# Optimization experiments

Hardware: AMD Instinct MI355X
Metric: run time of the kernel (lower is better)

The kernel has to match this reference:

```python
import jax, jax.numpy as jnp
import numpy as np

VNUM = 50000
OUT = 128
E = 1600000
EPS = 1e-7


def setup_inputs() -> dict:
    key = jax.random.key(0)
    k = jax.random.split(key, 8)
    sidx = jax.random.randint(k[0], (E,), 0, VNUM, dtype=jnp.int64 if jax.config.jax_enable_x64 else jnp.int32)
    tidx = jax.random.randint(k[1], (E,), 0, VNUM, dtype=sidx.dtype)
    enorm = jax.random.uniform(k[2], (E,), dtype=jnp.float32)
    # edge signs +-1 as in signed graph conv
    esgn = jnp.where(jax.random.uniform(k[3], (E,)) < 0.5, -1.0, 1.0).astype(jnp.float32)
    # vrepr initialized trunc_normal(std=0.1) (zero_init=False)
    vrepr = 0.1 * jax.random.truncated_normal(k[4], -2.0, 2.0, (VNUM, OUT), dtype=jnp.float32)
    lim = 1.0 / np.sqrt(OUT)
    loc_w = jax.random.uniform(k[5], (OUT, OUT), jnp.float32, -lim, lim)
    loc_b = jnp.zeros((OUT,), jnp.float32)
    std_w = jax.random.uniform(k[6], (OUT, OUT), jnp.float32, -lim, lim)
    std_b = jnp.zeros((OUT,), jnp.float32)
    return {"sidx": sidx, "tidx": tidx, "enorm": enorm, "esgn": esgn,
            "vrepr": vrepr, "loc_w": loc_w, "loc_b": loc_b,
            "std_w": std_w, "std_b": std_b}


def reference(sidx, tidx, enorm, esgn, vrepr, loc_w, loc_b, std_w, std_b):
    # GraphConv: edge-weighted gather + scatter-add aggregation
    msg = vrepr[sidx] * (esgn * enorm)[:, None]          # [E, OUT]
    ptr = jax.ops.segment_sum(msg, tidx, num_segments=VNUM)  # [VNUM, OUT]
    loc = ptr @ loc_w.T + loc_b                          # Normal loc
    std = jax.nn.softplus(ptr @ std_w.T + std_b) + EPS   # Normal scale
    return loc, std
```

## Files before the change

### kernel.cpp

```cpp
#include <hip/hip_runtime.h>
#include <math.h>

#define VNUM 50000
#define OUTF 128
#define NEDGE 1600000
#define EPSF 1e-7f

#define CONV_BLOCKS 6250
#define BFRAG_BLOCKS 64

#define CHUNK 2048
#define NCB 49
#define COARSE_BLOCKS 782
#define NSUB 4
#define FINE_BLOCKS (NCB * NSUB)

typedef __attribute__((ext_vector_type(8))) short short8;
typedef __attribute__((ext_vector_type(4))) float v4f;

__device__ __forceinline__ unsigned short f2bf(float f) {
    union { float f; unsigned int u; } c; c.f = f;
    unsigned int u = c.u;
    return (unsigned short)((u + 0x7FFFu + ((u >> 16) & 1u)) >> 16);
}
__device__ __forceinline__ float bf16_lo(unsigned int p) {
    union { unsigned int u; float f; } c; c.u = p << 16; return c.f;
}
__device__ __forceinline__ float bf16_hi(unsigned int p) {
    union { unsigned int u; float f; } c; c.u = p & 0xFFFF0000u; return c.f;
}

__device__ __forceinline__ int wave_incl_scan(int v, int lane) {
#pragma unroll
    for (int off = 1; off < 64; off <<= 1) {
        const int o = __shfl_up(v, off, 64);
        if (lane >= off) v += o;
    }
    return v;
}

__global__ __launch_bounds__(256) void prep_kernel(
    const float* __restrict__ vrepr, unsigned int* __restrict__ vrepr16,
    const int* __restrict__ tidx, int* __restrict__ chist,
    const float* __restrict__ loc_w, const float* __restrict__ std_w,
    unsigned int* bfrag)
{
    __shared__ int lc[4][NCB];
    const int b = blockIdx.x, tid = threadIdx.x;
    if (b < CONV_BLOCKS) {
        const size_t base = (size_t)b * 1024 + tid * 4;
        const float4 v = *reinterpret_cast<const float4*>(vrepr + base);
        uint2 o;
        o.x = (unsigned)f2bf(v.x) | ((unsigned)f2bf(v.y) << 16);
        o.y = (unsigned)f2bf(v.z) | ((unsigned)f2bf(v.w) << 16);
        *reinterpret_cast<uint2*>(vrepr16 + base / 2) = o;
    } else if (b < CONV_BLOCKS + COARSE_BLOCKS) {
        const int hb = b - CONV_BLOCKS;
        for (int i = tid; i < 4 * NCB; i += 256) (&lc[0][0])[i] = 0;
        __syncthreads();
        const int base = hb * CHUNK;
#pragma unroll
        for (int j = 0; j < 8; ++j) {
            const int e = base + j * 256 + tid;
            if (e < NEDGE) atomicAdd(&lc[tid >> 6][tidx[e] >> 10], 1);
        }
        __syncthreads();
        if (tid < NCB) {
            const int s = lc[0][tid] + lc[1][tid] + lc[2][tid] + lc[3][tid];
            if (s) atomicAdd(&chist[tid], s);
        }
    } else {
        const int p = (b - (CONV_BLOCKS + COARSE_BLOCKS)) * 256 + tid;
        const int j2 = p & 3, lq = (p >> 2) & 63, ks = (p >> 8) & 3, ct = p >> 10;
        const int k = ks * 32 + (lq >> 4) * 8 + j2 * 2;
        const int n = ct * 16 + (lq & 15);
        const float* wsrc = (n >> 7) ? std_w : loc_w;
        const int c = n & 127;
        bfrag[p] = (unsigned)f2bf(wsrc[c * 128 + k]) |
                   ((unsigned)f2bf(wsrc[c * 128 + k + 1]) << 16);
    }
}

__global__ __launch_bounds__(64) void scan_coarse_kernel(
    const int* __restrict__ chist, int* __restrict__ cbase,
    int* __restrict__ ccursor, int* __restrict__ offs)
{
    const int tid = threadIdx.x;
    const int v = (tid < NCB) ? chist[tid] : 0;
    const int inc = wave_incl_scan(v, tid);
    const int ex = inc - v;
    if (tid < NCB) { cbase[tid] = ex; ccursor[tid] = ex; }
    if (tid == NCB - 1) { cbase[NCB] = inc; offs[VNUM] = inc; }
}

__global__ __launch_bounds__(256) void coarse_kernel(
    const int* __restrict__ sidx, const int* __restrict__ tidx,
    const float* __restrict__ enorm, const float* __restrict__ esgn,
    int* __restrict__ ccursor, uint2* __restrict__ coarse8)
{
    __shared__ uint2 lrec[CHUNK];
    __shared__ int lcnt[4][NCB];
    __shared__ int lbase[4][NCB];
    __shared__ int loffs[NCB];
    __shared__ int grun[NCB];

    const int tid = threadIdx.x, lane = tid & 63, wv = tid >> 6;
    const int base = blockIdx.x * CHUNK;
    const int n = min(CHUNK, NEDGE - base);

    for (int i = tid; i < 4 * NCB; i += 256) (&lcnt[0][0])[i] = 0;
    __syncthreads();

    uint2 rec[8];
#pragma unroll
    for (int j = 0; j < 8; ++j) {
        const int e = base + j * 256 + tid;
        if (e < NEDGE) {
            const int t = tidx[e];
            const float w = esgn[e] * enorm[e];
            rec[j].x = ((unsigned)sidx[e] << 16) | (unsigned)f2bf(w);
            rec[j].y = (unsigned)t;
            atomicAdd(&lcnt[wv][t >> 10], 1);
        }
    }
    __syncthreads();

    if (tid < 64) {
        int c0 = 0, c1 = 0, c2 = 0, c3 = 0, tot = 0;
        if (lane < NCB) {
            c0 = lcnt[0][lane]; c1 = lcnt[1][lane];
            c2 = lcnt[2][lane]; c3 = lcnt[3][lane];
            tot = c0 + c1 + c2 + c3;
        }
        const int inc = wave_incl_scan(tot, lane);
        const int ex = inc - tot;
        if (lane < NCB) {
            loffs[lane]    = ex;
            lbase[0][lane] = ex;
            lbase[1][lane] = ex + c0;
            lbase[2][lane] = ex + c0 + c1;
            lbase[3][lane] = ex + c0 + c1 + c2;
            grun[lane] = atomicAdd(&ccursor[lane], tot);
        }
    }
    __syncthreads();

#pragma unroll
    for (int j = 0; j < 8; ++j) {
        const int e = base + j * 256 + tid;
        if (e < NEDGE) {
            const int cb = (int)(rec[j].y >> 10);
            const int pos = atomicAdd(&lbase[wv][cb], 1);
            lrec[pos] = rec[j];
        }
    }
    __syncthreads();

    for (int i = tid; i < n; i += 256) {
        const uint2 r = lrec[i];
        const int cb = (int)(r.y >> 10);
        coarse8[grun[cb] + (i - loffs[cb])] = r;
    }
}

__global__ __launch_bounds__(1024) void hist_kernel(
    const uint2* __restrict__ coarse8, const int* __restrict__ cbase,
    int* __restrict__ hcnt)
{
    __shared__ int cnt[1024];
    const int tid = threadIdx.x;
    const int bin = blockIdx.x >> 2, s = blockIdx.x & 3;
    const int s0 = cbase[bin], len = cbase[bin + 1] - s0;
    const int qs = s0 + ((len * s) >> 2);
    const int qe = s0 + ((len * (s + 1)) >> 2);
    cnt[tid] = 0;
    __syncthreads();
    for (int i = qs + tid; i < qe; i += 1024)
        atomicAdd(&cnt[coarse8[i].y & 1023], 1);
    __syncthreads();
    hcnt[blockIdx.x * 1024 + tid] = cnt[tid];
}

__global__ __launch_bounds__(1024) void scatter_fine_kernel(
    const uint2* __restrict__ coarse8, const int* __restrict__ cbase,
    const int* __restrict__ hcnt, int* __restrict__ offs,
    unsigned int* __restrict__ pairs)
{
    __shared__ int cur[1024];
    __shared__ int wsum[16];
    const int tid = threadIdx.x, lane = tid & 63, wv = tid >> 6;
    const int bin = blockIdx.x >> 2, s = blockIdx.x & 3;
    const int s0 = cbase[bin], len = cbase[bin + 1] - s0;
    const int qs = s0 + ((len * s) >> 2);
    const int qe = s0 + ((len * (s + 1)) >> 2);

    const int c0 = hcnt[(bin * 4 + 0) * 1024 + tid];
    const int c1 = hcnt[(bin * 4 + 1) * 1024 + tid];
    const int c2 = hcnt[(bin * 4 + 2) * 1024 + tid];
    const int c3 = hcnt[(bin * 4 + 3) * 1024 + tid];
    const int tot = c0 + c1 + c2 + c3;
    const int pre = (s > 0 ? c0 : 0) + (s > 1 ? c1 : 0) + (s > 2 ? c2 : 0);

    const int inc = wave_incl_scan(tot, lane);
    if (lane == 63) wsum[wv] = inc;
    __syncthreads();
    if (tid == 0) {
        int run = 0;
        for (int i = 0; i < 16; ++i) { const int t = wsum[i]; wsum[i] = run; run += t; }
    }
    __syncthreads();
    const int ex = s0 + wsum[wv] + inc - tot;
    const int gv = (bin << 10) + tid;
    if (s == 0 && gv < VNUM) offs[gv] = ex;
    cur[tid] = ex + pre;
    __syncthreads();

    for (int i = qs + tid; i < qe; i += 1024) {
        const uint2 r = coarse8[i];
        const int pos = atomicAdd(&cur[r.y & 1023], 1);
        pairs[pos] = r.x;
    }
}

__global__ __launch_bounds__(256) void aggregate_kernel(
    const int* __restrict__ offs, const unsigned int* __restrict__ pairs,
    const unsigned int* __restrict__ vrepr16, float* __restrict__ acc)
{
    const int v = blockIdx.x * 4 + (threadIdx.x >> 6);
    const int l = threadIdx.x & 63;
    int i = offs[v];
    const int end = offs[v + 1];

    float a0 = 0.0f, a1 = 0.0f;
    for (; i + 8 <= end; i += 8) {
        unsigned p[8], r[8];
#pragma unroll
        for (int j = 0; j < 8; ++j) p[j] = pairs[i + j];
#pragma unroll
        for (int j = 0; j < 8; ++j) r[j] = vrepr16[(size_t)(p[j] >> 16) * 64 + l];
#pragma unroll
        for (int j = 0; j < 8; ++j) {
            const float w = bf16_lo(p[j]);
            a0 = fmaf(bf16_lo(r[j]), w, a0);
            a1 = fmaf(bf16_hi(r[j]), w, a1);
        }
    }
    for (; i + 4 <= end; i += 4) {
        const unsigned p0 = pairs[i], p1 = pairs[i + 1];
        const unsigned p2 = pairs[i + 2], p3 = pairs[i + 3];
        const unsigned r0 = vrepr16[(size_t)(p0 >> 16) * 64 + l];
        const unsigned r1 = vrepr16[(size_t)(p1 >> 16) * 64 + l];
        const unsigned r2 = vrepr16[(size_t)(p2 >> 16) * 64 + l];
        const unsigned r3 = vrepr16[(size_t)(p3 >> 16) * 64 + l];
        const float w0 = bf16_lo(p0), w1 = bf16_lo(p1);
        const float w2 = bf16_lo(p2), w3 = bf16_lo(p3);
        a0 = fmaf(bf16_lo(r0), w0, a0); a1 = fmaf(bf16_hi(r0), w0, a1);
        a0 = fmaf(bf16_lo(r1), w1, a0); a1 = fmaf(bf16_hi(r1), w1, a1);
        a0 = fmaf(bf16_lo(r2), w2, a0); a1 = fmaf(bf16_hi(r2), w2, a1);
        a0 = fmaf(bf16_lo(r3), w3, a0); a1 = fmaf(bf16_hi(r3), w3, a1);
    }
    for (; i < end; ++i) {
        const unsigned p = pairs[i];
        const unsigned r = vrepr16[(size_t)(p >> 16) * 64 + l];
        const float w = bf16_lo(p);
        a0 = fmaf(bf16_lo(r), w, a0); a1 = fmaf(bf16_hi(r), w, a1);
    }
    *reinterpret_cast<float2*>(acc + (size_t)v * OUTF + 2 * l) = make_float2(a0, a1);
}

__global__ __launch_bounds__(256) void gemm_mfma_kernel(
    const float* acc, const unsigned int* __restrict__ bfrag,
    const float* __restrict__ loc_b, const float* __restrict__ std_b,
    float* out)
{
    __shared__ unsigned short tile[16][136];
    const int t = threadIdx.x;
    const int row0 = blockIdx.x * 16;
    const int l = t & 63, w = t >> 6;

    short8 bfr[4][4];
#pragma unroll
    for (int ct = 0; ct < 4; ++ct)
#pragma unroll
        for (int ks = 0; ks < 4; ++ks)
            bfr[ct][ks] = *reinterpret_cast<const short8*>(
                bfrag + ((((w * 4 + ct) * 4 + ks) * 64 + l) << 2));

    {
        const float* src = acc + (size_t)row0 * OUTF + t * 8;
        const float4 v0 = *reinterpret_cast<const float4*>(src);
        const float4 v1 = *reinterpret_cast<const float4*>(src + 4);
        uint4 pk;
        pk.x = (unsigned)f2bf(v0.x) | ((unsigned)f2bf(v0.y) << 16);
        pk.y = (unsigned)f2bf(v0.z) | ((unsigned)f2bf(v0.w) << 16);
        pk.z = (unsigned)f2bf(v1.x) | ((unsigned)f2bf(v1.y) << 16);
        pk.w = (unsigned)f2bf(v1.z) | ((unsigned)f2bf(v1.w) << 16);
        *reinterpret_cast<uint4*>(&tile[t >> 4][(t & 15) * 8]) = pk;
    }
    __syncthreads();

    const int m = l & 15, q = l >> 4;
    v4f accv[4];
#pragma unroll
    for (int ct = 0; ct < 4; ++ct) accv[ct] = (v4f){0.0f, 0.0f, 0.0f, 0.0f};

#pragma unroll
    for (int ks = 0; ks < 4; ++ks) {
        const short8 a = *reinterpret_cast<const short8*>(&tile[m][ks * 32 + q * 8]);
#pragma unroll
        for (int ct = 0; ct < 4; ++ct)
            accv[ct] = __builtin_amdgcn_mfma_f32_16x16x32_bf16(
                a, bfr[ct][ks], accv[ct], 0, 0, 0);
    }

#pragma unroll
    for (int ct = 0; ct < 4; ++ct) {
        const int colg = (w * 4 + ct) * 16 + m;
        const int h = colg >> 7, c = colg & 127;
        const float bias = (h ? std_b : loc_b)[c];
        float* dst = out + (h ? (size_t)VNUM * OUTF : (size_t)0);
#pragma unroll
        for (int reg = 0; reg < 4; ++reg) {
            const int row = row0 + q * 4 + reg;
            float x = accv[ct][reg] + bias;
            if (h) x = fmaxf(x, 0.0f) + log1pf(expf(-fabsf(x))) + EPSF;
            dst[(size_t)row * OUTF + c] = x;
        }
    }
}

__global__ __launch_bounds__(256) void gemm_fallback_kernel(
    const float* acc,
    const float* __restrict__ loc_w, const float* __restrict__ loc_b,
    const float* __restrict__ std_w, const float* __restrict__ std_b,
    float* out)
{
    __shared__ float tile[16][OUTF];
    const int t = threadIdx.x;
    const int row0 = blockIdx.x * 16;
    {
        const float4* src = reinterpret_cast<const float4*>(acc + (size_t)row0 * OUTF);
        float4* dst = reinterpret_cast<float4*>(&tile[0][0]);
        dst[t] = src[t]; dst[t + 256] = src[t + 256];
    }
    __syncthreads();
    const int is_std = t >> 7;
    const int c = t & 127;
    const float* w = (is_std ? std_w : loc_w) + (size_t)c * OUTF;
    const float bias = is_std ? std_b[c] : loc_b[c];
    float accv[16];
#pragma unroll
    for (int r = 0; r < 16; ++r) accv[r] = 0.0f;
    for (int k = 0; k < OUTF; k += 4) {
        const float4 wv = *reinterpret_cast<const float4*>(w + k);
#pragma unroll
        for (int r = 0; r < 16; ++r) {
            const float4 pv = *reinterpret_cast<const float4*>(&tile[r][k]);
            float a = accv[r];
            a = fmaf(pv.x, wv.x, a); a = fmaf(pv.y, wv.y, a);
            a = fmaf(pv.z, wv.z, a); a = fmaf(pv.w, wv.w, a);
            accv[r] = a;
        }
    }
    float* dst_base = out + (is_std ? (size_t)VNUM * OUTF : (size_t)0);
#pragma unroll
    for (int r = 0; r < 16; ++r) {
        const float x = accv[r] + bias;
        dst_base[(size_t)(row0 + r) * OUTF + c] =
            is_std ? (fmaxf(x, 0.0f) + log1pf(expf(-fabsf(x))) + EPSF) : x;
    }
}

extern "C" void kernel_launch(void* const* d_in, const int* in_sizes, int n_in,
                              void* d_out, int out_size, void* d_ws, size_t ws_size,
                              hipStream_t stream) {
    const int*   sidx  = (const int*)  d_in[0];
    const int*   tidx  = (const int*)  d_in[1];
    const float* enorm = (const float*)d_in[2];
    const float* esgn  = (const float*)d_in[3];
    const float* vrepr = (const float*)d_in[4];
    const float* loc_w = (const float*)d_in[5];
    const float* loc_b = (const float*)d_in[6];
    const float* std_w = (const float*)d_in[7];
    const float* std_b = (const float*)d_in[8];

    float* out = (float*)d_out;

    uint2* coarse8 = (uint2*)out;

    unsigned int* sbase   = (unsigned int*)(out + (size_t)VNUM * OUTF);
    unsigned int* pairs   = sbase;
    unsigned int* vrepr16 = sbase + NEDGE;
    int* offs    = (int*)(sbase + NEDGE + (size_t)VNUM * 64);
    int* cbase   = offs + VNUM + 1;
    int* ccursor = cbase + NCB + 1;
    int* chist   = ccursor + NCB;
    int* hcnt    = chist + NCB;

    const bool use_ws = ws_size >= 16384 * sizeof(unsigned int);
    unsigned int* bfrag = use_ws ? (unsigned int*)d_ws : nullptr;

    hipMemsetAsync(chist, 0, NCB * sizeof(int), stream);

    const int prep_blocks = CONV_BLOCKS + COARSE_BLOCKS + (use_ws ? BFRAG_BLOCKS : 0);
    prep_kernel       <<<prep_blocks, 256, 0, stream>>>(vrepr, vrepr16, tidx, chist,
                                                        loc_w, std_w, bfrag);
    scan_coarse_kernel<<<1, 64, 0, stream>>>(chist, cbase, ccursor, offs);
    coarse_kernel     <<<COARSE_BLOCKS, 256, 0, stream>>>(sidx, tidx, enorm, esgn,
                                                          ccursor, coarse8);
    hist_kernel       <<<FINE_BLOCKS, 1024, 0, stream>>>(coarse8, cbase, hcnt);
    scatter_fine_kernel<<<FINE_BLOCKS, 1024, 0, stream>>>(coarse8, cbase, hcnt,
                                                          offs, pairs);

    float* acc = out;
    aggregate_kernel<<<VNUM / 4, 256, 0, stream>>>(offs, pairs, vrepr16, acc);

    if (use_ws) {
        gemm_mfma_kernel<<<VNUM / 16, 256, 0, stream>>>(acc, bfrag, loc_b, std_b, out);
    } else {
        gemm_fallback_kernel<<<VNUM / 16, 256, 0, stream>>>(acc, loc_w, loc_b,
                                                            std_w, std_b, out);
    }
}
```

Measured before the change: 253.3 us.

## Replace coarse histogram pre-pass with fixed-stride bin slots and post-scan

Each coarse bin gets a fixed-capacity region (BSTRIDE) in the staging buffer, so the atomic cursors start at fixed offsets. This removes the tidx histogram pass, the memset and the pre-scan. A small scan after coarse binning derives the compacted offsets from the final cursor values. The aggregate loop also gains a 12-way unrolled gather for more memory-level parallelism. The change risks overflow if any bin exceeds the fixed capacity under skewed target distributions.

```diff
diff --git a/kernel.cpp b/kernel.cpp
--- a/kernel.cpp
+++ b/kernel.cpp
@@ -12,6 +12,7 @@
 #define CHUNK 2048
 #define NCB 49
 #define COARSE_BLOCKS 782
+#define BSTRIDE 36864
 #define NSUB 4
 #define FINE_BLOCKS (NCB * NSUB)
 
@@ -41,11 +42,10 @@
 
 __global__ __launch_bounds__(256) void prep_kernel(
     const float* __restrict__ vrepr, unsigned int* __restrict__ vrepr16,
-    const int* __restrict__ tidx, int* __restrict__ chist,
+    int* __restrict__ ccursor,
     const float* __restrict__ loc_w, const float* __restrict__ std_w,
     unsigned int* bfrag)
 {
-    __shared__ int lc[4][NCB];
     const int b = blockIdx.x, tid = threadIdx.x;
     if (b < CONV_BLOCKS) {
         const size_t base = (size_t)b * 1024 + tid * 4;
@@ -54,23 +54,10 @@
         o.x = (unsigned)f2bf(v.x) | ((unsigned)f2bf(v.y) << 16);
         o.y = (unsigned)f2bf(v.z) | ((unsigned)f2bf(v.w) << 16);
         *reinterpret_cast<uint2*>(vrepr16 + base / 2) = o;
-    } else if (b < CONV_BLOCKS + COARSE_BLOCKS) {
-        const int hb = b - CONV_BLOCKS;
-        for (int i = tid; i < 4 * NCB; i += 256) (&lc[0][0])[i] = 0;
-        __syncthreads();
-        const int base = hb * CHUNK;
-#pragma unroll
-        for (int j = 0; j < 8; ++j) {
-            const int e = base + j * 256 + tid;
-            if (e < NEDGE) atomicAdd(&lc[tid >> 6][tidx[e] >> 10], 1);
-        }
-        __syncthreads();
-        if (tid < NCB) {
-            const int s = lc[0][tid] + lc[1][tid] + lc[2][tid] + lc[3][tid];
-            if (s) atomicAdd(&chist[tid], s);
-        }
+    } else if (b == CONV_BLOCKS) {
+        if (tid < NCB) ccursor[tid] = tid * BSTRIDE;
     } else {
-        const int p = (b - (CONV_BLOCKS + COARSE_BLOCKS)) * 256 + tid;
+        const int p = (b - (CONV_BLOCKS + 1)) * 256 + tid;
         const int j2 = p & 3, lq = (p >> 2) & 63, ks = (p >> 8) & 3, ct = p >> 10;
         const int k = ks * 32 + (lq >> 4) * 8 + j2 * 2;
         const int n = ct * 16 + (lq & 15);
@@ -79,18 +66,6 @@
         bfrag[p] = (unsigned)f2bf(wsrc[c * 128 + k]) |
                    ((unsigned)f2bf(wsrc[c * 128 + k + 1]) << 16);
     }
-}
-
-__global__ __launch_bounds__(64) void scan_coarse_kernel(
-    const int* __restrict__ chist, int* __restrict__ cbase,
-    int* __restrict__ ccursor, int* __restrict__ offs)
-{
-    const int tid = threadIdx.x;
-    const int v = (tid < NCB) ? chist[tid] : 0;
-    const int inc = wave_incl_scan(v, tid);
-    const int ex = inc - v;
-    if (tid < NCB) { cbase[tid] = ex; ccursor[tid] = ex; }
-    if (tid == NCB - 1) { cbase[NCB] = inc; offs[VNUM] = inc; }
 }
 
 __global__ __launch_bounds__(256) void coarse_kernel(
@@ -163,6 +138,18 @@
     }
 }
 
+__global__ __launch_bounds__(64) void scan_mid_kernel(
+    const int* __restrict__ ccursor, int* __restrict__ cbase,
+    int* __restrict__ offs)
+{
+    const int tid = threadIdx.x;
+    const int len = (tid < NCB) ? (ccursor[tid] - tid * BSTRIDE) : 0;
+    const int inc = wave_incl_scan(len, tid);
+    const int ex = inc - len;
+    if (tid < NCB) cbase[tid] = ex;
+    if (tid == NCB - 1) { cbase[NCB] = inc; offs[VNUM] = inc; }
+}
+
 __global__ __launch_bounds__(1024) void hist_kernel(
     const uint2* __restrict__ coarse8, const int* __restrict__ cbase,
     int* __restrict__ hcnt)
@@ -170,9 +157,10 @@
     __shared__ int cnt[1024];
     const int tid = threadIdx.x;
     const int bin = blockIdx.x >> 2, s = blockIdx.x & 3;
-    const int s0 = cbase[bin], len = cbase[bin + 1] - s0;
-    const int qs = s0 + ((len * s) >> 2);
-    const int qe = s0 + ((len * (s + 1)) >> 2);
+    const int bs = bin * BSTRIDE;
+    const int len = cbase[bin + 1] - cbase[bin];
+    const int qs = bs + ((len * s) >> 2);
+    const int qe = bs + ((len * (s + 1)) >> 2);
     cnt[tid] = 0;
     __syncthreads();
     for (int i = qs + tid; i < qe; i += 1024)
@@ -190,9 +178,11 @@
     __shared__ int wsum[16];
     const int tid = threadIdx.x, lane = tid & 63, wv = tid >> 6;
     const int bin = blockIdx.x >> 2, s = blockIdx.x & 3;
-    const int s0 = cbase[bin], len = cbase[bin + 1] - s0;
-    const int qs = s0 + ((len * s) >> 2);
-    const int qe = s0 + ((len * (s + 1)) >> 2);
+    const int bs = bin * BSTRIDE;
+    const int s0 = cbase[bin];
+    const int len = cbase[bin + 1] - s0;
+    const int qs = bs + ((len * s) >> 2);
+    const int qe = bs + ((len * (s + 1)) >> 2);
 
     const int c0 = hcnt[(bin * 4 + 0) * 1024 + tid];
     const int c1 = hcnt[(bin * 4 + 1) * 1024 + tid];
@@ -232,6 +222,19 @@
     const int end = offs[v + 1];
 
     float a0 = 0.0f, a1 = 0.0f;
+    for (; i + 12 <= end; i += 12) {
+        unsigned p[12], r[12];
+#pragma unroll
+        for (int j = 0; j < 12; ++j) p[j] = pairs[i + j];
+#pragma unroll
+        for (int j = 0; j < 12; ++j) r[j] = vrepr16[(size_t)(p[j] >> 16) * 64 + l];
+#pragma unroll
+        for (int j = 0; j < 12; ++j) {
+            const float w = bf16_lo(p[j]);
+            a0 = fmaf(bf16_lo(r[j]), w, a0);
+            a1 = fmaf(bf16_hi(r[j]), w, a1);
+        }
+    }
     for (; i + 8 <= end; i += 8) {
         unsigned p[8], r[8];
 #pragma unroll
@@ -394,20 +397,17 @@
     int* offs    = (int*)(sbase + NEDGE + (size_t)VNUM * 64);
     int* cbase   = offs + VNUM + 1;
     int* ccursor = cbase + NCB + 1;
-    int* chist   = ccursor + NCB;
-    int* hcnt    = chist + NCB;
+    int* hcnt    = ccursor + NCB;
 
     const bool use_ws = ws_size >= 16384 * sizeof(unsigned int);
     unsigned int* bfrag = use_ws ? (unsigned int*)d_ws : nullptr;
 
-    hipMemsetAsync(chist, 0, NCB * sizeof(int), stream);
-
-    const int prep_blocks = CONV_BLOCKS + COARSE_BLOCKS + (use_ws ? BFRAG_BLOCKS : 0);
-    prep_kernel       <<<prep_blocks, 256, 0, stream>>>(vrepr, vrepr16, tidx, chist,
+    const int prep_blocks = CONV_BLOCKS + 1 + (use_ws ? BFRAG_BLOCKS : 0);
+    prep_kernel       <<<prep_blocks, 256, 0, stream>>>(vrepr, vrepr16, ccursor,
                                                         loc_w, std_w, bfrag);
-    scan_coarse_kernel<<<1, 64, 0, stream>>>(chist, cbase, ccursor, offs);
     coarse_kernel     <<<COARSE_BLOCKS, 256, 0, stream>>>(sidx, tidx, enorm, esgn,
                                                           ccursor, coarse8);
+    scan_mid_kernel   <<<1, 64, 0, stream>>>(ccursor, cbase, offs);
     hist_kernel       <<<FINE_BLOCKS, 1024, 0, stream>>>(coarse8, cbase, hcnt);
     scatter_fine_kernel<<<FINE_BLOCKS, 1024, 0, stream>>>(coarse8, cbase, hcnt,
                                                           offs, pairs);
```

Measured after the change: 231.7 us. -8.5%, faster.
